# Performance work log

Measured on AMD Instinct MI355X. Metric: run time of the kernel, lower is better.

Reference implementation:

```python
import jax, jax.numpy as jnp
import numpy as np

N_HEADS = 16
MASK_NEG = -1e32


def setup_inputs() -> dict:
    key = jax.random.key(0)
    k0, k1, k2, k3, k4 = jax.random.split(key, 5)
    B, S, D = 8, 1024, 1024
    return {
        "q": jax.random.normal(k0, (B, S, D), dtype=jnp.float32),
        "k": jax.random.normal(k1, (B, S, D), dtype=jnp.float32),
        "v1": jax.random.normal(k2, (B, S, D), dtype=jnp.float32),
        "v2": jax.random.normal(k3, (B, S, D), dtype=jnp.float32),
        "counter_attention_mask": jax.random.randint(k4, (B, S), 0, 2, dtype=jnp.int32),
    }


def reference(q, k, v1, v2, counter_attention_mask):
    B, S, D = q.shape
    H = N_HEADS
    dk = D // H

    def split_heads(x):
        return x.reshape(B, S, H, dk).transpose(0, 2, 1, 3)  # [B,H,S,dk]

    qh, kh, v1h, v2h = split_heads(q), split_heads(k), split_heads(v1), split_heads(v2)

    # scaled dot-product scores [B,H,S,S]
    scores = jnp.einsum("bhqd,bhkd->bhqk", qh, kh) / jnp.sqrt(jnp.float32(dk))

    # create_mask(input, 0): allowed only where key_idx < query_idx (strict causal)
    i = jnp.arange(S)[:, None]
    j = jnp.arange(S)[None, :]
    allowed = j < i  # [S,S]
    scores = jnp.where(allowed[None, None], scores, MASK_NEG)

    # first softmax
    p = jax.nn.softmax(scores, axis=-1)

    # counter-attention mask: zero out masked key columns (per batch, all heads/rows)
    cm = counter_attention_mask[:, None, None, :]  # [B,1,1,S]
    p = jnp.where(cm == 1, jnp.float32(0.0), p)

    # second softmax over the (partially zeroed) probabilities
    p = jax.nn.softmax(p, axis=-1)

    # zero the first query row (pad_zero concat in the original)
    p = p.at[:, :, 0, :].set(0.0)

    out1 = jnp.einsum("bhqk,bhkd->bhqd", p, v1h)
    out2 = jnp.einsum("bhqk,bhkd->bhqd", p, v2h)

    def merge_heads(x):
        return x.transpose(0, 2, 1, 3).reshape(B, S, D)

    return merge_heads(out1), merge_heads(out2)
```

## Files before the change

kernel.cpp:

```cpp
#include <hip/hip_runtime.h>
#include <hip/hip_bf16.h>

#define B_ 8
#define S_ 1024
#define D_ 1024
#define H_ 16
#define DK_ 64
#define BH_ (B_ * H_)

typedef float f32x4 __attribute__((ext_vector_type(4)));
typedef short s16x8 __attribute__((ext_vector_type(8)));
typedef short s16x4 __attribute__((ext_vector_type(4)));

#define EXP2F(x) __builtin_amdgcn_exp2f(x)
#define LOG2F(x) __builtin_amdgcn_logf(x)
#define LOG2E 1.44269504088896f

static __device__ __forceinline__ short f2b(float f) {
  unsigned u = __builtin_bit_cast(unsigned, f);
  u = u + 0x7FFFu + ((u >> 16) & 1u);
  return (short)(u >> 16);
}
static __device__ __forceinline__ short f2bn(float f) {
  __hip_bfloat16 h = __float2bfloat16(f);
  return __builtin_bit_cast(short, h);
}

static __device__ __forceinline__ int slotf(int g, int e) {
  return (e < 4) ? (4 * g + e) : (16 + 4 * g + (e - 4));
}


__global__ __launch_bounds__(256) void prep_k(const float* __restrict__ k,
                                              short* __restrict__ kb) {
  const int bid = blockIdx.x;
  const int s0 = (bid & 63) * 16;
  const int b = bid >> 6;
  const int tid = threadIdx.x;
#pragma unroll
  for (int it = 0; it < 8; ++it) {
    int li = it * 256 + tid;
    int s = s0 + (li >> 7);
    int ch = li & 127;
    int h = ch >> 3;
    int dk0 = (ch & 7) * 8;
    const float* src = k + ((size_t)(b * S_ + s)) * D_ + ch * 8;
    s16x8 o;
#pragma unroll
    for (int e = 0; e < 8; ++e) o[e] = f2b(src[e]);
    *(s16x8*)(kb + ((size_t)((b * H_ + h) * S_ + s)) * DK_ + dk0) = o;
  }
}

__global__ __launch_bounds__(256) void prep_v(const float* __restrict__ v1,
                                              const float* __restrict__ v2,
                                              short* __restrict__ v1f,
                                              short* __restrict__ v2f,
                                              float* __restrict__ vs) {
  const int bid = blockIdx.x;
  const int sg = bid & 3;
  const int h = (bid >> 2) & 15;
  const int b = bid >> 6;
  const int tid = threadIdx.x;
  const int db = tid >> 6;
  const int lane = tid & 63;
  const int r = lane & 15;
  const int g = lane >> 4;
  const size_t inbase = (size_t)b * S_ * D_ + h * DK_ + db * 16 + r;
  float s1 = 0.f, s2 = 0.f;
#pragma unroll
  for (int it = 0; it < 8; ++it) {
    int jt = sg * 8 + it;
    int j0 = jt * 32;
    s16x8 o1, o2;
#pragma unroll
    for (int e = 0; e < 8; ++e) {
      int j = j0 + slotf(g, e);
      float a = v1[inbase + (size_t)j * D_];
      float c = v2[inbase + (size_t)j * D_];
      s1 += a;
      s2 += c;
      o1[e] = f2b(a);
      o2[e] = f2b(c);
    }
    size_t off = (((size_t)((b * H_ + h) * 32 + jt) * 4 + db) * 64 + lane) * 8;
    *(s16x8*)(v1f + off) = o1;
    *(s16x8*)(v2f + off) = o2;
  }
  s1 += __shfl_xor(s1, 16);
  s1 += __shfl_xor(s1, 32);
  s2 += __shfl_xor(s2, 16);
  s2 += __shfl_xor(s2, 32);
  if (g == 0) {
    int dd = db * 16 + r;
    atomicAdd(&vs[(size_t)b * D_ + h * DK_ + dd], s1);
    atomicAdd(&vs[(size_t)(B_ + b) * D_ + h * DK_ + dd], s2);
  }
}

__global__ __launch_bounds__(256, 2) void attn_fast7(
    const float* __restrict__ q, const short* __restrict__ kb,
    const short* __restrict__ v1f, const short* __restrict__ v2f,
    const int* __restrict__ cm, const float* __restrict__ vs,
    float* __restrict__ out) {
  const int bid = blockIdx.x;
  const int xcd = bid & 7;
  const int idx = bid >> 3;
  const int pr = idx & 7;
  const int bhgrp = idx >> 3;
  const int bh = bhgrp * 8 + xcd;
  const int b = bh >> 4, h = bh & 15;

  const int tid = threadIdx.x;
  const int wid = tid >> 6;
  const int lane = tid & 63;
  const int r = lane & 15;
  const int g = lane >> 4;

  const int aseg = 8 + pr;
  const int bseg = 7 - pr;
  const int qh = aseg * 64 + wid * 16;
  const int ql = bseg * 64 + (3 - wid) * 16;
  const int iqh = qh + r;
  const int iql = ql + r;
  const int njt = aseg + 1;

  __shared__ __align__(16) char sbuf[2][24576];
  __shared__ unsigned cmw[32];
  {
    const int* cmb = cm + b * S_;
#pragma unroll
    for (int it = 0; it < 4; ++it) {
      unsigned long long m = __ballot(cmb[it * 256 + tid] == 1);
      if (lane == 0) {
        int w0 = it * 8 + wid * 2;
        cmw[w0] = (unsigned)m;
        cmw[w0 + 1] = (unsigned)(m >> 32);
      }
    }
  }

  const float qscale = 0.125f * LOG2E;
  s16x8 qfh0, qfh1, qfl0, qfl1;
  {
    const float* qp = q + ((size_t)(b * S_ + qh + r)) * D_ + h * DK_;
#pragma unroll
    for (int e = 0; e < 8; ++e) qfh0[e] = f2bn(qp[8 * g + e] * qscale);
#pragma unroll
    for (int e = 0; e < 8; ++e) qfh1[e] = f2bn(qp[32 + 8 * g + e] * qscale);
    const float* qp2 = q + ((size_t)(b * S_ + ql + r)) * D_ + h * DK_;
#pragma unroll
    for (int e = 0; e < 8; ++e) qfl0[e] = f2bn(qp2[8 * g + e] * qscale);
#pragma unroll
    for (int e = 0; e < 8; ++e) qfl1[e] = f2bn(qp2[32 + 8 * g + e] * qscale);
  }

  const short* kbh = kb + (size_t)bh * S_ * DK_;
  const short* v1bh = v1f + (size_t)bh * 32 * 2048;
  const short* v2bh = v2f + (size_t)bh * 32 * 2048;

  const int r0s = tid >> 3, c0s = tid & 7;
  const int r1s = (tid + 256) >> 3, c1s = tid & 7;

#define SLK(g0, g1, jtv)                                          \
  {                                                               \
    const short* kp = kbh + (size_t)(jtv) * 4096;                 \
    g0 = *(const s16x8*)(kp + tid * 8);                           \
    g1 = *(const s16x8*)(kp + (tid + 256) * 8);                   \
  }
#define SWK(buf, g0, g1)                                          \
  {                                                               \
    *(s16x8*)((buf) + r0s * 128 + ((c0s ^ (r0s & 7)) * 16)) = g0; \
    *(s16x8*)((buf) + r1s * 128 + ((c1s ^ (r1s & 7)) * 16)) = g1; \
  }
#define SLV(a0, a1, b0, b1, jtv)                                  \
  {                                                               \
    const short* p1 = v1bh + (size_t)(jtv) * 4096;                \
    const short* p2 = v2bh + (size_t)(jtv) * 4096;                \
    a0 = *(const s16x8*)(p1 + tid * 8);                           \
    a1 = *(const s16x8*)(p1 + (tid + 256) * 8);                   \
    b0 = *(const s16x8*)(p2 + tid * 8);                           \
    b1 = *(const s16x8*)(p2 + (tid + 256) * 8);                   \
  }
#define SWV(buf, a0, a1, b0, b1)                                  \
  {                                                               \
    *(s16x8*)((buf) + 8192 + tid * 16) = a0;                      \
    *(s16x8*)((buf) + 8192 + (tid + 256) * 16) = a1;              \
    *(s16x8*)((buf) + 16384 + tid * 16) = b0;                     \
    *(s16x8*)((buf) + 16384 + (tid + 256) * 16) = b1;             \
  }
#define KFRAG(sK, row, quad) \
  (*(const s16x8*)((sK) + (row)*128 + (((quad) ^ ((row)&7)) * 16)))

  float Zh = 0.f, Zl = 0.f;
  {
    s16x8 rk0, rk1;
    SLK(rk0, rk1, 0);
    __syncthreads();
    SWK(sbuf[0], rk0, rk1);
    __syncthreads();
    for (int jt = 0; jt < njt; ++jt) {
      const char* sK = sbuf[jt & 1];
      const bool pf = (jt + 1 < njt);
      s16x8 nk0, nk1;
      if (pf) SLK(nk0, nk1, jt + 1);
      const bool chB = (jt == aseg);
      const bool clB = (jt == bseg);
#pragma unroll
      for (int sub = 0; sub < 2; ++sub) {
        const int jsb = jt * 64 + sub * 32;
        const int row0 = sub * 32 + r, row1 = row0 + 16;
        s16x8 k00 = KFRAG(sK, row0, g);
        s16x8 k01 = KFRAG(sK, row0, 4 + g);
        s16x8 k10 = KFRAG(sK, row1, g);
        s16x8 k11 = KFRAG(sK, row1, 4 + g);
        f32x4 s0 = {0.f, 0.f, 0.f, 0.f}, s1 = {0.f, 0.f, 0.f, 0.f};
        s0 = __builtin_amdgcn_mfma_f32_16x16x32_bf16(k00, qfh0, s0, 0, 0, 0);
        s0 = __builtin_amdgcn_mfma_f32_16x16x32_bf16(k01, qfh1, s0, 0, 0, 0);
        s1 = __builtin_amdgcn_mfma_f32_16x16x32_bf16(k10, qfh0, s1, 0, 0, 0);
        s1 = __builtin_amdgcn_mfma_f32_16x16x32_bf16(k11, qfh1, s1, 0, 0, 0);
        if (chB) {
#pragma unroll
          for (int e = 0; e < 4; ++e) {
            int j0 = jsb + 4 * g + e, j1 = jsb + 16 + 4 * g + e;
            Zh += (j0 < iqh) ? EXP2F(s0[e]) : 0.f;
            Zh += (j1 < iqh) ? EXP2F(s1[e]) : 0.f;
          }
        } else {
#pragma unroll
          for (int e = 0; e < 4; ++e) Zh += EXP2F(s0[e]) + EXP2F(s1[e]);
        }
        if (jsb < ql + 16) {
          f32x4 t0 = {0.f, 0.f, 0.f, 0.f}, t1 = {0.f, 0.f, 0.f, 0.f};
          t0 = __builtin_amdgcn_mfma_f32_16x16x32_bf16(k00, qfl0, t0, 0, 0, 0);
          t0 = __builtin_amdgcn_mfma_f32_16x16x32_bf16(k01, qfl1, t0, 0, 0, 0);
          t1 = __builtin_amdgcn_mfma_f32_16x16x32_bf16(k10, qfl0, t1, 0, 0, 0);
          t1 = __builtin_amdgcn_mfma_f32_16x16x32_bf16(k11, qfl1, t1, 0, 0, 0);
          if (clB) {
#pragma unroll
            for (int e = 0; e < 4; ++e) {
              int j0 = jsb + 4 * g + e, j1 = jsb + 16 + 4 * g + e;
              Zl += (j0 < iql) ? EXP2F(t0[e]) : 0.f;
              Zl += (j1 < iql) ? EXP2F(t1[e]) : 0.f;
            }
          } else {
#pragma unroll
            for (int e = 0; e < 4; ++e) Zl += EXP2F(t0[e]) + EXP2F(t1[e]);
          }
        }
      }
      if (pf) SWK(sbuf[(jt + 1) & 1], nk0, nk1);
      __syncthreads();
    }
  }
  Zh += __shfl_xor(Zh, 16);
  Zh += __shfl_xor(Zh, 32);
  Zl += __shfl_xor(Zl, 16);
  Zl += __shfl_xor(Zl, 32);
  const float lzh = -LOG2F(Zh);
  const float lzl = -LOG2F(Zl);

  f32x4 a1h[4], a2h[4], a1l[4], a2l[4];
#pragma unroll
  for (int d0 = 0; d0 < 4; ++d0) {
    a1h[d0] = (f32x4){0.f, 0.f, 0.f, 0.f};
    a2h[d0] = (f32x4){0.f, 0.f, 0.f, 0.f};
    a1l[d0] = (f32x4){0.f, 0.f, 0.f, 0.f};
    a2l[d0] = (f32x4){0.f, 0.f, 0.f, 0.f};
  }
  f32x4 wsh = {0.f, 0.f, 0.f, 0.f}, wsl = {0.f, 0.f, 0.f, 0.f};
  s16x8 ones;
#pragma unroll
  for (int e = 0; e < 8; ++e) ones[e] = (short)0x3F80;

  {
    s16x8 rk0, rk1, ra0, ra1, rb0, rb1;
    SLK(rk0, rk1, 0);
    SLV(ra0, ra1, rb0, rb1, 0);
    SWK(sbuf[0], rk0, rk1);
    SWV(sbuf[0], ra0, ra1, rb0, rb1);
    __syncthreads();
    for (int jt = 0; jt < njt; ++jt) {
      const char* sB = sbuf[jt & 1];
      const bool pf = (jt + 1 < njt);
      s16x8 nk0, nk1, na0, na1, nb0, nb1;
      if (pf) {
        SLK(nk0, nk1, jt + 1);
        SLV(na0, na1, nb0, nb1, jt + 1);
      }
      const bool chB = (jt == aseg);
      const bool clB = (jt == bseg);
#pragma unroll
      for (int sub = 0; sub < 2; ++sub) {
        const int jsb = jt * 64 + sub * 32;
        const int row0 = sub * 32 + r, row1 = row0 + 16;
        s16x8 k00 = KFRAG(sB, row0, g);
        s16x8 k01 = KFRAG(sB, row0, 4 + g);
        s16x8 k10 = KFRAG(sB, row1, g);
        s16x8 k11 = KFRAG(sB, row1, 4 + g);
        f32x4 s0 = {0.f, 0.f, 0.f, 0.f}, s1 = {0.f, 0.f, 0.f, 0.f};
        s0 = __builtin_amdgcn_mfma_f32_16x16x32_bf16(k00, qfh0, s0, 0, 0, 0);
        s0 = __builtin_amdgcn_mfma_f32_16x16x32_bf16(k01, qfh1, s0, 0, 0, 0);
        s1 = __builtin_amdgcn_mfma_f32_16x16x32_bf16(k10, qfh0, s1, 0, 0, 0);
        s1 = __builtin_amdgcn_mfma_f32_16x16x32_bf16(k11, qfh1, s1, 0, 0, 0);
        const bool bc = (jsb < ql + 16);
        f32x4 t0, t1;
        if (bc) {
          t0 = (f32x4){0.f, 0.f, 0.f, 0.f};
          t1 = (f32x4){0.f, 0.f, 0.f, 0.f};
          t0 = __builtin_amdgcn_mfma_f32_16x16x32_bf16(k00, qfl0, t0, 0, 0, 0);
          t0 = __builtin_amdgcn_mfma_f32_16x16x32_bf16(k01, qfl1, t0, 0, 0, 0);
          t1 = __builtin_amdgcn_mfma_f32_16x16x32_bf16(k10, qfl0, t1, 0, 0, 0);
          t1 = __builtin_amdgcn_mfma_f32_16x16x32_bf16(k11, qfl1, t1, 0, 0, 0);
        }
        const unsigned cw = cmw[2 * jt + sub];
        int cmbit[8];
#pragma unroll
        for (int s2 = 0; s2 < 2; ++s2)
#pragma unroll
          for (int e = 0; e < 4; ++e)
            cmbit[s2 * 4 + e] = (int)((cw >> (s2 * 16 + 4 * g + e)) & 1u);
        s16x8 wah;
        {
          float wv[8];
#pragma unroll
          for (int s2 = 0; s2 < 2; ++s2) {
            f32x4 sv = s2 ? s1 : s0;
#pragma unroll
            for (int e = 0; e < 4; ++e) {
              int j = jsb + s2 * 16 + 4 * g + e;
              float pe = EXP2F(sv[e] + lzh);
              float xe = EXP2F(pe * LOG2E) - 1.f;
              bool ok = !cmbit[s2 * 4 + e];
              if (chB) ok = ok && (j < iqh);
              wv[s2 * 4 + e] = ok ? xe : 0.f;
            }
          }
#pragma unroll
          for (int e = 0; e < 8; ++e) wah[e] = f2bn(wv[e]);
        }
        s16x8 wal;
        if (bc) {
          float wv[8];
#pragma unroll
          for (int s2 = 0; s2 < 2; ++s2) {
            f32x4 sv = s2 ? t1 : t0;
#pragma unroll
            for (int e = 0; e < 4; ++e) {
              int j = jsb + s2 * 16 + 4 * g + e;
              float pe = EXP2F(sv[e] + lzl);
              float xe = EXP2F(pe * LOG2E) - 1.f;
              bool ok = !cmbit[s2 * 4 + e];
              if (clB) ok = ok && (j < iql);
              wv[s2 * 4 + e] = ok ? xe : 0.f;
            }
          }
#pragma unroll
          for (int e = 0; e < 8; ++e) wal[e] = f2bn(wv[e]);
        }
        const char* vb1p = sB + 8192 + sub * 4096;
        const char* vb2p = sB + 16384 + sub * 4096;
        s16x8 vb1[4], vb2[4];
#pragma unroll
        for (int db = 0; db < 4; ++db) {
          vb1[db] = *(const s16x8*)(vb1p + (db * 64 + lane) * 16);
          vb2[db] = *(const s16x8*)(vb2p + (db * 64 + lane) * 16);
        }
#pragma unroll
        for (int db = 0; db < 4; ++db) {
          a1h[db] = __builtin_amdgcn_mfma_f32_16x16x32_bf16(wah, vb1[db], a1h[db], 0, 0, 0);
          a2h[db] = __builtin_amdgcn_mfma_f32_16x16x32_bf16(wah, vb2[db], a2h[db], 0, 0, 0);
        }
        wsh = __builtin_amdgcn_mfma_f32_16x16x32_bf16(wah, ones, wsh, 0, 0, 0);
        if (bc) {
#pragma unroll
          for (int db = 0; db < 4; ++db) {
            a1l[db] = __builtin_amdgcn_mfma_f32_16x16x32_bf16(wal, vb1[db], a1l[db], 0, 0, 0);
            a2l[db] = __builtin_amdgcn_mfma_f32_16x16x32_bf16(wal, vb2[db], a2l[db], 0, 0, 0);
          }
          wsl = __builtin_amdgcn_mfma_f32_16x16x32_bf16(wal, ones, wsl, 0, 0, 0);
        }
      }
      if (pf) {
        SWK(sbuf[(jt + 1) & 1], nk0, nk1);
        SWV(sbuf[(jt + 1) & 1], na0, na1, nb0, nb1);
      }
      __syncthreads();
    }
  }
#undef SLK
#undef SLV
#undef SWK
#undef SWV
#undef KFRAG

  float* out1 = out;
  float* out2 = out + (size_t)B_ * S_ * D_;
  const float* vs1 = vs + (size_t)b * D_ + h * DK_;
  const float* vs2 = vs + (size_t)(B_ + b) * D_ + h * DK_;

#pragma unroll
  for (int e = 0; e < 4; ++e) {
    {
      float inv = 1.f / ((float)S_ + wsh[e]);
      int io = qh + 4 * g + e;
      size_t ro = ((size_t)(b * S_) + io) * D_ + h * DK_;
#pragma unroll
      for (int db = 0; db < 4; ++db) {
        int dd = db * 16 + r;
        out1[ro + dd] = (a1h[db][e] + vs1[dd]) * inv;
        out2[ro + dd] = (a2h[db][e] + vs2[dd]) * inv;
      }
    }
    {
      float inv = 1.f / ((float)S_ + wsl[e]);
      int io = ql + 4 * g + e;
      bool zero = (io == 0);
      size_t ro = ((size_t)(b * S_) + io) * D_ + h * DK_;
#pragma unroll
      for (int db = 0; db < 4; ++db) {
        int dd = db * 16 + r;
        out1[ro + dd] = zero ? 0.f : (a1l[db][e] + vs1[dd]) * inv;
        out2[ro + dd] = zero ? 0.f : (a2l[db][e] + vs2[dd]) * inv;
      }
    }
  }
}


__global__ __launch_bounds__(256) void vsum_kernel(const float* __restrict__ v1,
                                                   const float* __restrict__ v2,
                                                   float* __restrict__ vs) {
  int bid = blockIdx.x;
  int sc = bid & 7, dc = (bid >> 3) & 3, b = bid >> 5;
  int d = dc * 256 + threadIdx.x;
  const float* p1 = v1 + ((size_t)b * S_ + sc * 128) * D_ + d;
  const float* p2 = v2 + ((size_t)b * S_ + sc * 128) * D_ + d;
  float s1 = 0.f, s2 = 0.f;
  for (int j = 0; j < 128; ++j) {
    s1 += p1[(size_t)j * D_];
    s2 += p2[(size_t)j * D_];
  }
  atomicAdd(&vs[b * D_ + d], s1);
  atomicAdd(&vs[B_ * D_ + b * D_ + d], s2);
}

__global__ __launch_bounds__(256) void dualattn_fallback(
    const float* __restrict__ q, const float* __restrict__ k,
    const float* __restrict__ v1, const float* __restrict__ v2,
    const int* __restrict__ cm, const float* __restrict__ vs,
    float* __restrict__ out) {
  const int bid = blockIdx.x;
  const int qt = bid & 15;
  const int h = (bid >> 4) & 15;
  const int b = bid >> 8;
  const int tid = threadIdx.x;
  const int wid = tid >> 6;
  const int lane = tid & 63;
  const int r = lane & 15;
  const int g = lane >> 4;
  const int qw = qt * 64 + wid * 16;
  const int iq = qw + r;

  __shared__ __align__(16) char kbuf[32 * 128];
  __shared__ __align__(16) char vtb1[64 * 64];
  __shared__ __align__(16) char vtb2[64 * 64];
  __shared__ unsigned cmw[32];

  {
    const int* cmb = cm + b * S_;
#pragma unroll
    for (int it = 0; it < 4; ++it) {
      int c = cmb[it * 256 + tid];
      unsigned long long m = __ballot(c == 1);
      if (lane == 0) {
        int w0 = (it * 256 + wid * 64) >> 5;
        cmw[w0] = (unsigned)m;
        cmw[w0 + 1] = (unsigned)(m >> 32);
      }
    }
  }

  s16x8 qf0, qf1;
  {
    const float* qp = q + ((size_t)(b * S_) + qw + r) * D_ + h * DK_;
#pragma unroll
    for (int e = 0; e < 8; ++e) qf0[e] = f2b(qp[8 * g + e] * 0.125f);
#pragma unroll
    for (int e = 0; e < 8; ++e) qf1[e] = f2b(qp[32 + 8 * g + e] * 0.125f);
  }

  const int njt = 2 * qt + 2;
  const float* kbase = k + (size_t)(b * S_) * D_ + h * DK_;
  const float* v1base = v1 + (size_t)(b * S_) * D_ + h * DK_;
  const float* v2base = v2 + (size_t)(b * S_) * D_ + h * DK_;
  const int srow = tid >> 3;
  const int sch = tid & 7;

  float m1 = -INFINITY, Z1 = 0.f;
  for (int jt = 0; jt < njt; ++jt) {
    const int jbase = jt * 32;
    __syncthreads();
    {
      const float* kr = kbase + (size_t)(jbase + srow) * D_ + sch * 8;
      s16x8 pk;
#pragma unroll
      for (int e = 0; e < 8; ++e) pk[e] = f2b(kr[e]);
      *(s16x8*)(kbuf + srow * 128 + ((sch ^ (srow & 7)) * 16)) = pk;
    }
    __syncthreads();
    if (jbase < qw + 16) {
#pragma unroll
      for (int sub = 0; sub < 2; ++sub) {
        const int jsb = jbase + sub * 16;
        if (jsb < qw + 16) {
          const int row = sub * 16 + r;
          s16x8 ka0 = *(const s16x8*)(kbuf + row * 128 + ((g ^ (row & 7)) * 16));
          s16x8 ka1 = *(const s16x8*)(kbuf + row * 128 + (((4 + g) ^ (row & 7)) * 16));
          f32x4 sv = {0.f, 0.f, 0.f, 0.f};
          sv = __builtin_amdgcn_mfma_f32_16x16x32_bf16(ka0, qf0, sv, 0, 0, 0);
          sv = __builtin_amdgcn_mfma_f32_16x16x32_bf16(ka1, qf1, sv, 0, 0, 0);
          float tm = m1;
#pragma unroll
          for (int e = 0; e < 4; ++e) {
            int j = jsb + 4 * g + e;
            if (j < iq) tm = fmaxf(tm, sv[e]);
          }
          if (tm > m1) { Z1 *= __expf(m1 - tm); m1 = tm; }
#pragma unroll
          for (int e = 0; e < 4; ++e) {
            int j = jsb + 4 * g + e;
            if (j < iq) Z1 += __expf(sv[e] - tm);
          }
        }
      }
    }
  }
#pragma unroll
  for (int off = 16; off < 64; off <<= 1) {
    float mo = __shfl_xor(m1, off);
    float zo = __shfl_xor(Z1, off);
    float mn = fmaxf(m1, mo);
    if (mn > -INFINITY) {
      Z1 = Z1 * __expf(m1 - mn) + zo * __expf(mo - mn);
      m1 = mn;
    }
  }
  float z1i;
  if (m1 > -INFINITY) { z1i = 1.f / Z1; }
  else { z1i = 0.f; m1 = 0.f; }

  f32x4 acc1[4], acc2[4];
#pragma unroll
  for (int d0 = 0; d0 < 4; ++d0) {
    acc1[d0] = (f32x4){0.f, 0.f, 0.f, 0.f};
    acc2[d0] = (f32x4){0.f, 0.f, 0.f, 0.f};
  }
  float wsum = 0.f;

  for (int jt = 0; jt < njt; ++jt) {
    const int jbase = jt * 32;
    __syncthreads();
    {
      const float* kr = kbase + (size_t)(jbase + srow) * D_ + sch * 8;
      s16x8 pk;
#pragma unroll
      for (int e = 0; e < 8; ++e) pk[e] = f2b(kr[e]);
      *(s16x8*)(kbuf + srow * 128 + ((sch ^ (srow & 7)) * 16)) = pk;
      const float* v1r = v1base + (size_t)(jbase + srow) * D_ + sch * 8;
      const float* v2r = v2base + (size_t)(jbase + srow) * D_ + sch * 8;
#pragma unroll
      for (int e = 0; e < 8; ++e) {
        int dd = sch * 8 + e;
        int off = dd * 64 + (((srow >> 2) ^ (dd & 7)) * 8) + (srow & 3) * 2;
        *(short*)(vtb1 + off) = f2b(v1r[e]);
        *(short*)(vtb2 + off) = f2b(v2r[e]);
      }
    }
    __syncthreads();
    if (jbase < qw + 16) {
      const unsigned cmword = cmw[jbase >> 5];
      float w[8];
#pragma unroll
      for (int sub = 0; sub < 2; ++sub) {
        const int jsb = jbase + sub * 16;
        if (jsb < qw + 16) {
          const int row = sub * 16 + r;
          s16x8 ka0 = *(const s16x8*)(kbuf + row * 128 + ((g ^ (row & 7)) * 16));
          s16x8 ka1 = *(const s16x8*)(kbuf + row * 128 + (((4 + g) ^ (row & 7)) * 16));
          f32x4 sv = {0.f, 0.f, 0.f, 0.f};
          sv = __builtin_amdgcn_mfma_f32_16x16x32_bf16(ka0, qf0, sv, 0, 0, 0);
          sv = __builtin_amdgcn_mfma_f32_16x16x32_bf16(ka1, qf1, sv, 0, 0, 0);
#pragma unroll
          for (int e = 0; e < 4; ++e) {
            int j = jsb + 4 * g + e;
            float x = 0.f;
            if (j < iq && !((cmword >> (j & 31)) & 1u)) {
              float p = __expf(sv[e] - m1) * z1i;
              x = __expf(p) - 1.f;
            }
            w[sub * 4 + e] = x;
            wsum += x;
          }
        } else {
#pragma unroll
          for (int e = 0; e < 4; ++e) w[sub * 4 + e] = 0.f;
        }
      }
      s16x8 wa;
#pragma unroll
      for (int e = 0; e < 8; ++e) wa[e] = f2b(w[e]);
#pragma unroll
      for (int db = 0; db < 4; ++db) {
        const int dd = db * 16 + r;
        const int off0 = dd * 64 + ((g ^ (dd & 7)) * 8);
        const int off1 = dd * 64 + (((4 + g) ^ (dd & 7)) * 8);
        s16x4 lo1 = *(const s16x4*)(vtb1 + off0);
        s16x4 hi1 = *(const s16x4*)(vtb1 + off1);
        s16x8 vb1 = __builtin_shufflevector(lo1, hi1, 0, 1, 2, 3, 4, 5, 6, 7);
        acc1[db] = __builtin_amdgcn_mfma_f32_16x16x32_bf16(wa, vb1, acc1[db], 0, 0, 0);
        s16x4 lo2 = *(const s16x4*)(vtb2 + off0);
        s16x4 hi2 = *(const s16x4*)(vtb2 + off1);
        s16x8 vb2 = __builtin_shufflevector(lo2, hi2, 0, 1, 2, 3, 4, 5, 6, 7);
        acc2[db] = __builtin_amdgcn_mfma_f32_16x16x32_bf16(wa, vb2, acc2[db], 0, 0, 0);
      }
    }
  }

  wsum += __shfl_xor(wsum, 16);
  wsum += __shfl_xor(wsum, 32);
  const float z2 = (float)S_ + wsum;

  float* out1 = out;
  float* out2 = out + (size_t)B_ * S_ * D_;
#pragma unroll
  for (int e = 0; e < 4; ++e) {
    float z2e = __shfl(z2, 4 * g + e);
    float inv = 1.f / z2e;
    int io = qw + 4 * g + e;
    bool zero = (io == 0);
    size_t ro = ((size_t)(b * S_) + io) * D_ + h * DK_;
#pragma unroll
    for (int db = 0; db < 4; ++db) {
      int dd = db * 16 + r;
      float c1 = vs[(size_t)b * D_ + h * DK_ + dd];
      float c2 = vs[(size_t)(B_ + b) * D_ + h * DK_ + dd];
      out1[ro + dd] = zero ? 0.f : (acc1[db][e] + c1) * inv;
      out2[ro + dd] = zero ? 0.f : (acc2[db][e] + c2) * inv;
    }
  }
}


extern "C" void kernel_launch(void* const* d_in, const int* in_sizes, int n_in,
                              void* d_out, int out_size, void* d_ws, size_t ws_size,
                              hipStream_t stream) {
  (void)in_sizes; (void)n_in; (void)out_size;
  const float* q = (const float*)d_in[0];
  const float* k = (const float*)d_in[1];
  const float* v1 = (const float*)d_in[2];
  const float* v2 = (const float*)d_in[3];
  const int* cm = (const int*)d_in[4];
  float* outp = (float*)d_out;

  const size_t VS_BYTES = 2 * B_ * D_ * sizeof(float);
  const size_t FRAG_SHORTS = (size_t)BH_ * S_ * DK_;
  const size_t FRAG_BYTES = FRAG_SHORTS * 2;
  const size_t NEED = VS_BYTES + 3 * FRAG_BYTES;

  float* vs = (float*)d_ws;
  (void)hipMemsetAsync(vs, 0, VS_BYTES, stream);

  if (ws_size >= NEED) {
    short* kb = (short*)((char*)d_ws + VS_BYTES);
    short* v1f = kb + FRAG_SHORTS;
    short* v2f = v1f + FRAG_SHORTS;
    prep_k<<<B_ * (S_ / 16), 256, 0, stream>>>(k, kb);
    prep_v<<<B_ * H_ * 4, 256, 0, stream>>>(v1, v2, v1f, v2f, vs);
    attn_fast7<<<1024, 256, 0, stream>>>(q, kb, v1f, v2f, cm, vs, outp);
  } else {
    vsum_kernel<<<256, 256, 0, stream>>>(v1, v2, vs);
    dualattn_fallback<<<B_ * H_ * 16, 256, 0, stream>>>(q, k, v1, v2, cm, vs, outp);
  }
}
```

Measured before the change: 108.9 us.

## Stage K/V tiles directly into shared memory to raise occupancy to three blocks per CU

Global-to-shared staging now happens at the top of each tile iteration: the next tile is loaded and written to the alternate LDS buffer immediately, instead of being held in registers until the compute finishes. This frees the prefetch registers, which lets the launch bound move from 2 to 3 blocks per SM/CU. The block-to-work mapping is also reversed so that the heavier query pairs are scheduled first. The cost is that load latency is no longer hidden behind the MFMA work within a wave, so overlap now has to come from the extra resident waves, and the tighter register cap may cause spills.

```diff
diff --git a/kernel.cpp b/kernel.cpp
--- a/kernel.cpp
+++ b/kernel.cpp
@@ -98,7 +98,7 @@
   }
 }
 
-__global__ __launch_bounds__(256, 2) void attn_fast7(
+__global__ __launch_bounds__(256, 3) void attn_fast8(
     const float* __restrict__ q, const short* __restrict__ kb,
     const short* __restrict__ v1f, const short* __restrict__ v2f,
     const int* __restrict__ cm, const float* __restrict__ vs,
@@ -106,7 +106,7 @@
   const int bid = blockIdx.x;
   const int xcd = bid & 7;
   const int idx = bid >> 3;
-  const int pr = idx & 7;
+  const int pr = 7 - (idx & 7);
   const int bhgrp = idx >> 3;
   const int bh = bhgrp * 8 + xcd;
   const int b = bh >> 4, h = bh & 15;
@@ -162,48 +162,38 @@
   const int r0s = tid >> 3, c0s = tid & 7;
   const int r1s = (tid + 256) >> 3, c1s = tid & 7;
 
-#define SLK(g0, g1, jtv)                                          \
-  {                                                               \
-    const short* kp = kbh + (size_t)(jtv) * 4096;                 \
-    g0 = *(const s16x8*)(kp + tid * 8);                           \
-    g1 = *(const s16x8*)(kp + (tid + 256) * 8);                   \
-  }
-#define SWK(buf, g0, g1)                                          \
-  {                                                               \
-    *(s16x8*)((buf) + r0s * 128 + ((c0s ^ (r0s & 7)) * 16)) = g0; \
-    *(s16x8*)((buf) + r1s * 128 + ((c1s ^ (r1s & 7)) * 16)) = g1; \
-  }
-#define SLV(a0, a1, b0, b1, jtv)                                  \
-  {                                                               \
-    const short* p1 = v1bh + (size_t)(jtv) * 4096;                \
-    const short* p2 = v2bh + (size_t)(jtv) * 4096;                \
-    a0 = *(const s16x8*)(p1 + tid * 8);                           \
-    a1 = *(const s16x8*)(p1 + (tid + 256) * 8);                   \
-    b0 = *(const s16x8*)(p2 + tid * 8);                           \
-    b1 = *(const s16x8*)(p2 + (tid + 256) * 8);                   \
-  }
-#define SWV(buf, a0, a1, b0, b1)                                  \
-  {                                                               \
-    *(s16x8*)((buf) + 8192 + tid * 16) = a0;                      \
-    *(s16x8*)((buf) + 8192 + (tid + 256) * 16) = a1;              \
-    *(s16x8*)((buf) + 16384 + tid * 16) = b0;                     \
-    *(s16x8*)((buf) + 16384 + (tid + 256) * 16) = b1;             \
+#define STAGEK(buf, jtv)                                            \
+  {                                                                 \
+    const short* kp = kbh + (size_t)(jtv) * 4096;                   \
+    s16x8 g0 = *(const s16x8*)(kp + tid * 8);                       \
+    s16x8 g1 = *(const s16x8*)(kp + (tid + 256) * 8);               \
+    *(s16x8*)((buf) + r0s * 128 + ((c0s ^ (r0s & 7)) * 16)) = g0;   \
+    *(s16x8*)((buf) + r1s * 128 + ((c1s ^ (r1s & 7)) * 16)) = g1;   \
+  }
+#define STAGEV(buf, jtv)                                            \
+  {                                                                 \
+    const short* p1 = v1bh + (size_t)(jtv) * 4096;                  \
+    const short* p2 = v2bh + (size_t)(jtv) * 4096;                  \
+    s16x8 a0 = *(const s16x8*)(p1 + tid * 8);                       \
+    s16x8 a1 = *(const s16x8*)(p1 + (tid + 256) * 8);               \
+    s16x8 b0 = *(const s16x8*)(p2 + tid * 8);                       \
+    s16x8 b1 = *(const s16x8*)(p2 + (tid + 256) * 8);               \
+    *(s16x8*)((buf) + 8192 + tid * 16) = a0;                        \
+    *(s16x8*)((buf) + 8192 + (tid + 256) * 16) = a1;                \
+    *(s16x8*)((buf) + 16384 + tid * 16) = b0;                       \
+    *(s16x8*)((buf) + 16384 + (tid + 256) * 16) = b1;               \
   }
 #define KFRAG(sK, row, quad) \
   (*(const s16x8*)((sK) + (row)*128 + (((quad) ^ ((row)&7)) * 16)))
 
   float Zh = 0.f, Zl = 0.f;
   {
-    s16x8 rk0, rk1;
-    SLK(rk0, rk1, 0);
     __syncthreads();
-    SWK(sbuf[0], rk0, rk1);
+    STAGEK(sbuf[0], 0);
     __syncthreads();
     for (int jt = 0; jt < njt; ++jt) {
       const char* sK = sbuf[jt & 1];
-      const bool pf = (jt + 1 < njt);
-      s16x8 nk0, nk1;
-      if (pf) SLK(nk0, nk1, jt + 1);
+      if (jt + 1 < njt) STAGEK(sbuf[(jt + 1) & 1], jt + 1);
       const bool chB = (jt == aseg);
       const bool clB = (jt == bseg);
 #pragma unroll
@@ -249,7 +239,6 @@
           }
         }
       }
-      if (pf) SWK(sbuf[(jt + 1) & 1], nk0, nk1);
       __syncthreads();
     }
   }
@@ -274,19 +263,14 @@
   for (int e = 0; e < 8; ++e) ones[e] = (short)0x3F80;
 
   {
-    s16x8 rk0, rk1, ra0, ra1, rb0, rb1;
-    SLK(rk0, rk1, 0);
-    SLV(ra0, ra1, rb0, rb1, 0);
-    SWK(sbuf[0], rk0, rk1);
-    SWV(sbuf[0], ra0, ra1, rb0, rb1);
+    STAGEK(sbuf[0], 0);
+    STAGEV(sbuf[0], 0);
     __syncthreads();
     for (int jt = 0; jt < njt; ++jt) {
       const char* sB = sbuf[jt & 1];
-      const bool pf = (jt + 1 < njt);
-      s16x8 nk0, nk1, na0, na1, nb0, nb1;
-      if (pf) {
-        SLK(nk0, nk1, jt + 1);
-        SLV(na0, na1, nb0, nb1, jt + 1);
+      if (jt + 1 < njt) {
+        STAGEK(sbuf[(jt + 1) & 1], jt + 1);
+        STAGEV(sbuf[(jt + 1) & 1], jt + 1);
       }
       const bool chB = (jt == aseg);
       const bool clB = (jt == bseg);
@@ -381,17 +365,11 @@
           wsl = __builtin_amdgcn_mfma_f32_16x16x32_bf16(wal, ones, wsl, 0, 0, 0);
         }
       }
-      if (pf) {
-        SWK(sbuf[(jt + 1) & 1], nk0, nk1);
-        SWV(sbuf[(jt + 1) & 1], na0, na1, nb0, nb1);
-      }
       __syncthreads();
     }
   }
-#undef SLK
-#undef SLV
-#undef SWK
-#undef SWV
+#undef STAGEK
+#undef STAGEV
 #undef KFRAG
 
   float* out1 = out;
@@ -677,7 +655,7 @@
     short* v2f = v1f + FRAG_SHORTS;
     prep_k<<<B_ * (S_ / 16), 256, 0, stream>>>(k, kb);
     prep_v<<<B_ * H_ * 4, 256, 0, stream>>>(v1, v2, v1f, v2f, vs);
-    attn_fast7<<<1024, 256, 0, stream>>>(q, kb, v1f, v2f, cm, vs, outp);
+    attn_fast8<<<1024, 256, 0, stream>>>(q, kb, v1f, v2f, cm, vs, outp);
   } else {
     vsum_kernel<<<256, 256, 0, stream>>>(v1, v2, vs);
     dualattn_fallback<<<B_ * H_ * 16, 256, 0, stream>>>(q, k, v1, v2, cm, vs, outp);
```

New measurement: 125.4 us. 15.2% more time.
